# Kernel tuning notes

Measured on AMD Instinct MI355X. Metric: run time of the kernel, lower is better.

The kernel has to match this reference:

```python
import jax, jax.numpy as jnp
import numpy as np

# Model dims (match init_kwargs)
H = 16        # num query heads
HKV = 4       # num key/value heads
D = 128       # head dim
HID = H * D   # hidden size = 2048
W = 4         # ring world size; we simulate rank W-1 (sees all kv shards)
SL = 2048     # local (per-rank) sequence length


def _block_attn(q, kb, vb, scale, causal):
    # q: [B,H,Sl,D], kb/vb: [B,H,Sl,D]
    S = jnp.einsum('bhqd,bhkd->bhqk', q, kb) * scale
    if causal:
        mask = jnp.triu(jnp.ones((q.shape[2], kb.shape[2]), dtype=bool), k=1)
        S = jnp.where(mask[None, None], -jnp.inf, S)
    S_max = jnp.max(S, axis=-1, keepdims=True)
    exp_S = jnp.exp(S - S_max)
    exp_sum = jnp.sum(exp_S, axis=-1, keepdims=True)
    lse = jnp.log(exp_sum) + S_max            # [B,H,Sl,1]
    O = jnp.einsum('bhqk,bhkd->bhqd', exp_S / exp_sum, vb)
    return O, lse


def _ring_attention_fwd(x_q, x_kv, Wq, Wk, Wv, Wo):
    B, Sl, hid = x_q.shape
    n_rep = H // HKV
    scale = 1.0 / np.sqrt(D).astype(np.float32)

    q = (x_q @ Wq.T).reshape(B, Sl, H, D).transpose(0, 2, 1, 3)          # [B,H,Sl,D]
    k = (x_kv @ Wk.T).reshape(B, -1, HKV, D).transpose(0, 2, 1, 3)       # [B,Hkv,Stot,D]
    v = (x_kv @ Wv.T).reshape(B, -1, HKV, D).transpose(0, 2, 1, 3)
    # repeat_kv (GQA)
    k = jnp.repeat(k, n_rep, axis=1)                                     # [B,H,Stot,D]
    v = jnp.repeat(v, n_rep, axis=1)
    # split kv into W ring shards along sequence
    kb = k.reshape(B, H, W, Sl, D)
    vb = v.reshape(B, H, W, Sl, D)

    out, lse = None, None
    rank = W - 1
    for step in range(W):  # fixed small ring loop
        blk = rank - step  # shard held at this ring step (own shard first)
        bo, blse = _block_attn(q, kb[:, :, blk], vb[:, :, blk], scale, causal=(step == 0))
        if out is None:
            out, lse = bo, blse
        else:
            # online merge (matches update_out_and_lse)
            out = out - jax.nn.sigmoid(blse - lse) * (out - bo)
            lse = lse - jax.nn.log_sigmoid(lse - blse)

    out = out.transpose(0, 2, 1, 3).reshape(B, Sl, H * D)
    return out @ Wo.T


def setup_inputs() -> dict:
    key = jax.random.key(0)
    ks = jax.random.split(key, 6)
    s = 0.02
    return {
        'x_q': jax.random.normal(ks[0], (1, SL, HID), dtype=jnp.float32),
        'x_kv': jax.random.normal(ks[1], (1, W * SL, HID), dtype=jnp.float32),
        'Wq': jax.random.normal(ks[2], (HID, HID), dtype=jnp.float32) * s,
        'Wk': jax.random.normal(ks[3], (HKV * D, HID), dtype=jnp.float32) * s,
        'Wv': jax.random.normal(ks[4], (HKV * D, HID), dtype=jnp.float32) * s,
        'Wo': jax.random.normal(ks[5], (HID, HID), dtype=jnp.float32) * s,
    }


def reference(x_q, x_kv, Wq, Wk, Wv, Wo):
    return _ring_attention_fwd(x_q, x_kv, Wq, Wk, Wv, Wo)
```

## Files before the change

kernel.cpp:

```cpp
#include <hip/hip_runtime.h>
#include <stdint.h>

typedef unsigned short u16;
typedef short bf16x8 __attribute__((ext_vector_type(8)));
typedef float f32x4 __attribute__((ext_vector_type(4)));

#define MFMA16(a, b, c) __builtin_amdgcn_mfma_f32_16x16x32_bf16(a, b, c, 0, 0, 0)

__device__ __forceinline__ void ld_lds16(const void* g, void* l) {
  __builtin_amdgcn_global_load_lds(
      (const __attribute__((address_space(1))) void*)(uint64_t)(uintptr_t)g,
      (__attribute__((address_space(3))) void*)(uint32_t)(uintptr_t)l,
      16, 0, 0);
}

__device__ __forceinline__ u16 f32_to_bf16(float f) {
  uint32_t u = __float_as_uint(f);
  return (u16)((u + 0x7FFFu + ((u >> 16) & 1u)) >> 16);
}

__device__ __forceinline__ uint32_t cvt_pk_bf16(float a, float b) {
  uint32_t r;
  asm("v_cvt_pk_bf16_f32 %0, %1, %2" : "=v"(r) : "v"(a), "v"(b));
  return r;
}

__global__ void cvt_all(const float* __restrict__ xq, const float* __restrict__ xkv,
                        const float* __restrict__ Wq, const float* __restrict__ Wk,
                        const float* __restrict__ Wv, const float* __restrict__ Wo,
                        u16* __restrict__ xq_b, u16* __restrict__ xkv_b,
                        u16* __restrict__ wq_b, u16* __restrict__ wk_b,
                        u16* __restrict__ wv_b, u16* __restrict__ wo_b) {
  const int M4 = 1 << 20;
  const int total = 7 * M4 + (M4 >> 1);
  int i = blockIdx.x * blockDim.x + threadIdx.x;
  int stride = gridDim.x * blockDim.x;
  for (; i < total; i += stride) {
    const float* src;
    u16* dst;
    int off;
    if (i < M4)                         { src = xq;  dst = xq_b;  off = i; }
    else if (i < 5 * M4)                { src = xkv; dst = xkv_b; off = i - M4; }
    else if (i < 6 * M4)                { src = Wq;  dst = wq_b;  off = i - 5 * M4; }
    else if (i < 6 * M4 + (M4 >> 2))    { src = Wk;  dst = wk_b;  off = i - 6 * M4; }
    else if (i < 6 * M4 + (M4 >> 1))    { src = Wv;  dst = wv_b;  off = i - 6 * M4 - (M4 >> 2); }
    else                                { src = Wo;  dst = wo_b;  off = i - 6 * M4 - (M4 >> 1); }
    float4 v = reinterpret_cast<const float4*>(src)[off];
    ushort4 o;
    o.x = f32_to_bf16(v.x); o.y = f32_to_bf16(v.y);
    o.z = f32_to_bf16(v.z); o.w = f32_to_bf16(v.w);
    reinterpret_cast<ushort4*>(dst)[off] = o;
  }
}

__device__ __forceinline__ void gemm_body(const u16* __restrict__ A,
                                          const u16* __restrict__ B,
                                          void* __restrict__ Cv, int M, int N,
                                          int K, float alpha, int bx, int by,
                                          int outf32, u16* lA, u16* lB) {
  const int tid = threadIdx.x;
  const int lane = tid & 63;
  const int w = tid >> 6;
  const int c = lane & 15, g = lane >> 4;
  const int wm = (w & 1) * 64, wn = (w >> 1) * 32;
  const int m0 = by * 128, n0 = bx * 64;
  const int sr = tid >> 3, sc = tid & 7;

  f32x4 acc[4][2] = {};

  for (int k0 = 0; k0 < K; k0 += 64) {
    __syncthreads();
#pragma unroll
    for (int p = 0; p < 4; ++p) {
      int row = p * 32 + sr;
      int gc = sc ^ (row & 7);
      ld_lds16(A + (size_t)(m0 + row) * K + k0 + gc * 8, &lA[row * 64 + sc * 8]);
    }
#pragma unroll
    for (int p = 0; p < 2; ++p) {
      int idx = p * 256 + tid;
      int row = idx >> 3, cc = idx & 7;
      int gc = cc ^ (row & 7);
      ld_lds16(B + (size_t)(n0 + row) * K + k0 + gc * 8, &lB[row * 64 + cc * 8]);
    }
    __syncthreads();
#pragma unroll
    for (int kc = 0; kc < 2; ++kc) {
      bf16x8 a[4], b[2];
#pragma unroll
      for (int t = 0; t < 4; ++t) {
        int row = wm + t * 16 + c;
        int ch = (g + 4 * kc) ^ (row & 7);
        a[t] = *(const bf16x8*)&lA[row * 64 + ch * 8];
      }
#pragma unroll
      for (int t = 0; t < 2; ++t) {
        int row = wn + t * 16 + c;
        int ch = (g + 4 * kc) ^ (row & 7);
        b[t] = *(const bf16x8*)&lB[row * 64 + ch * 8];
      }
#pragma unroll
      for (int i = 0; i < 4; ++i)
#pragma unroll
        for (int j = 0; j < 2; ++j)
          acc[i][j] = MFMA16(a[i], b[j], acc[i][j]);
    }
  }

#pragma unroll
  for (int i = 0; i < 4; ++i)
#pragma unroll
    for (int j = 0; j < 2; ++j)
#pragma unroll
      for (int r = 0; r < 4; ++r) {
        int mm = m0 + wm + i * 16 + g * 4 + r;
        int nn = n0 + wn + j * 16 + c;
        float v = acc[i][j][r] * alpha;
        if (outf32)
          ((float*)Cv)[(size_t)mm * N + nn] = v;
        else
          ((u16*)Cv)[(size_t)mm * N + nn] = f32_to_bf16(v);
      }
}

__global__ __launch_bounds__(256, 4)
void gemm3(const u16* __restrict__ xq_b, const u16* __restrict__ wq_b,
           u16* __restrict__ Qb, const u16* __restrict__ xkv_b,
           const u16* __restrict__ wk_b, u16* __restrict__ Kb,
           const u16* __restrict__ wv_b, u16* __restrict__ VTb, float qscale) {
  __shared__ u16 lA[128 * 64];
  __shared__ u16 lB[64 * 64];
  int b = blockIdx.x;
  if (b < 512) {
    gemm_body(xq_b, wq_b, Qb, 2048, 2048, 2048, qscale, b & 31, b >> 5, 0, lA, lB);
  } else if (b < 1024) {
    b -= 512;
    gemm_body(xkv_b, wk_b, Kb, 8192, 512, 2048, 1.0f, b & 7, b >> 3, 0, lA, lB);
  } else {
    b -= 1024;
    gemm_body(wv_b, xkv_b, VTb, 512, 8192, 2048, 1.0f, b & 127, b >> 7, 0, lA, lB);
  }
}

__global__ __launch_bounds__(256, 4)
void gemm_out(const u16* __restrict__ A, const u16* __restrict__ B,
              float* __restrict__ Cv) {
  __shared__ u16 lA[128 * 64];
  __shared__ u16 lB[64 * 64];
  gemm_body(A, B, Cv, 2048, 2048, 2048, 1.0f, blockIdx.x, blockIdx.y, 1, lA, lB);
}

__global__ __launch_bounds__(256, 2)
void attn_kernel(const u16* __restrict__ Q, const u16* __restrict__ Kg,
                 const u16* __restrict__ VT, float* __restrict__ Opart,
                 float* __restrict__ mlp) {
  __shared__ u16 lK[2][64 * 128];
  __shared__ u16 lV[2][128 * 64];
  __shared__ uint32_t lP32[4][16 * 36];

  const int tid = threadIdx.x;
  const int w = tid >> 6, lane = tid & 63;
  const int c = lane & 15, g = lane >> 4;
  const int bx = blockIdx.x;
  const int h = bx & 15, qb = (bx >> 4) & 15, kvs = bx >> 8;
  const int hk = h >> 2;
  const int i0 = qb * 128;
  const int q0 = i0 + w * 32;

  const int nt = ((i0 + 6271) >> 6) + 1;
  const int nth = nt >> 1;
  const int t0 = kvs ? nth : 0;
  const int ntt = (kvs ? nt : nth) - t0;

  bf16x8 qf0[4], qf1[4];
#pragma unroll
  for (int kc = 0; kc < 4; ++kc) {
    qf0[kc] = *(const bf16x8*)&Q[(size_t)(q0 + c) * 2048 + h * 128 + kc * 32 + g * 8];
    qf1[kc] = *(const bf16x8*)&Q[(size_t)(q0 + 16 + c) * 2048 + h * 128 + kc * 32 + g * 8];
  }

  f32x4 a0[8] = {}, a1[8] = {};
  float m0s = -1e30f, l0s = 0.f, m1s = -1e30f, l1s = 0.f;

  auto stage = [&](int buf, int t) {
    const int j0 = t << 6;
#pragma unroll
    for (int p = 0; p < 4; ++p) {
      int idx = p * 256 + tid;
      int row = idx >> 4, cc = idx & 15;
      int gc = cc ^ (row & 15);
      ld_lds16(Kg + (size_t)(j0 + row) * 512 + hk * 128 + gc * 8,
               &lK[buf][row * 128 + cc * 8]);
    }
#pragma unroll
    for (int p = 0; p < 4; ++p) {
      int idx = p * 256 + tid;
      int row = idx >> 3, cc = idx & 7;
      int gc = cc ^ (row & 7);
      ld_lds16(VT + (size_t)(hk * 128 + row) * 8192 + j0 + gc * 8,
               &lV[buf][row * 64 + cc * 8]);
    }
  };

  uint32_t* lPw = &lP32[w][0];

  auto softmax_pb = [&](f32x4 (&sm)[4], float& ms, float& ls, f32x4 (&av)[8],
                        bf16x8 (&pb)[2]) {
    float tm = sm[0][0];
#pragma unroll
    for (int jt = 0; jt < 4; ++jt)
#pragma unroll
      for (int r = 0; r < 4; ++r) tm = fmaxf(tm, sm[jt][r]);
    tm = fmaxf(tm, __shfl_xor(tm, 16));
    tm = fmaxf(tm, __shfl_xor(tm, 32));
    if (!__all(tm - ms <= 8.0f)) {
      float mnew = fmaxf(ms, tm);
      float al = exp2f(ms - mnew);
      ls *= al; ms = mnew;
#pragma unroll
      for (int dt = 0; dt < 8; ++dt) av[dt] *= al;
    }
    float p_[4][4];
    float ps = 0.f;
#pragma unroll
    for (int jt = 0; jt < 4; ++jt)
#pragma unroll
      for (int r = 0; r < 4; ++r) {
        p_[jt][r] = exp2f(sm[jt][r] - ms);
        ps += p_[jt][r];
      }
    ps += __shfl_xor(ps, 16);
    ps += __shfl_xor(ps, 32);
    ls += ps;
#pragma unroll
    for (int jt = 0; jt < 4; ++jt) {
      lPw[c * 36 + jt * 8 + g * 2 + 0] = cvt_pk_bf16(p_[jt][0], p_[jt][1]);
      lPw[c * 36 + jt * 8 + g * 2 + 1] = cvt_pk_bf16(p_[jt][2], p_[jt][3]);
    }
    pb[0] = *(const bf16x8*)&lPw[c * 36 + g * 4];
    pb[1] = *(const bf16x8*)&lPw[c * 36 + 16 + g * 4];
  };

  stage(0, t0);

  for (int it = 0; it < ntt; ++it) {
    const int curb = it & 1;
    const int j0 = (t0 + it) << 6;
    if (it + 1 < ntt) {
      stage(curb ^ 1, t0 + it + 1);
      asm volatile("s_waitcnt vmcnt(8)" ::: "memory");
    } else {
      asm volatile("s_waitcnt vmcnt(0)" ::: "memory");
    }
    __builtin_amdgcn_s_barrier();

    f32x4 s0[4] = {}, s1[4] = {};
    __builtin_amdgcn_s_setprio(1);
#pragma unroll
    for (int kc = 0; kc < 4; ++kc)
#pragma unroll
      for (int jt = 0; jt < 4; ++jt) {
        int row = jt * 16 + c;
        int ch = (g + 4 * kc) ^ (row & 15);
        bf16x8 kf = *(const bf16x8*)&lK[curb][row * 128 + ch * 8];
        s0[jt] = MFMA16(kf, qf0[kc], s0[jt]);
        s1[jt] = MFMA16(kf, qf1[kc], s1[jt]);
      }
    __builtin_amdgcn_s_setprio(0);

    if (j0 + 63 > q0 + 6144) {
#pragma unroll
      for (int jt = 0; jt < 4; ++jt)
#pragma unroll
        for (int r = 0; r < 4; ++r) {
          int jg = j0 + jt * 16 + g * 4 + r;
          if (jg > q0 + c + 6144) s0[jt][r] = -1e30f;
          if (jg > q0 + 16 + c + 6144) s1[jt][r] = -1e30f;
        }
    }

    bf16x8 pb0[2], pb1[2];
    softmax_pb(s0, m0s, l0s, a0, pb0);
    softmax_pb(s1, m1s, l1s, a1, pb1);

    __builtin_amdgcn_s_setprio(1);
#pragma unroll
    for (int dt = 0; dt < 8; ++dt)
#pragma unroll
      for (int kc2 = 0; kc2 < 2; ++kc2) {
        int row = dt * 16 + c;
        int vch = (g + 4 * kc2) ^ (row & 7);
        bf16x8 vf = *(const bf16x8*)&lV[curb][row * 64 + vch * 8];
        a0[dt] = MFMA16(vf, pb0[kc2], a0[dt]);
        a1[dt] = MFMA16(vf, pb1[kc2], a1[dt]);
      }
    __builtin_amdgcn_s_setprio(0);

    __builtin_amdgcn_s_barrier();
  }

  const size_t pbase = ((size_t)(kvs * 16 + h) * 16 + qb);
  float* Op = Opart + pbase * 16384;
  float* mlb = mlp + pbase * 256;
  const int qi0 = w * 32 + c;
#pragma unroll
  for (int dt = 0; dt < 8; ++dt) {
    *(f32x4*)&Op[(size_t)qi0 * 128 + dt * 16 + g * 4] = a0[dt];
    *(f32x4*)&Op[(size_t)(qi0 + 16) * 128 + dt * 16 + g * 4] = a1[dt];
  }
  if (g == 0) {
    mlb[qi0] = m0s;
    mlb[128 + qi0] = l0s;
    mlb[qi0 + 16] = m1s;
    mlb[128 + qi0 + 16] = l1s;
  }
}

__global__ __launch_bounds__(256)
void attn_merge(const float* __restrict__ Opart, const float* __restrict__ mlp,
                u16* __restrict__ O) {
  const int bx = blockIdx.x;
  const int h = bx >> 4, qb = bx & 15;
  const int q = threadIdx.x & 127, hf = threadIdx.x >> 7;
  const size_t p0 = ((size_t)(0 + h) * 16 + qb);
  const size_t p1 = ((size_t)(16 + h) * 16 + qb);
  float mm0 = mlp[p0 * 256 + q], ll0 = mlp[p0 * 256 + 128 + q];
  float mm1 = mlp[p1 * 256 + q], ll1 = mlp[p1 * 256 + 128 + q];
  float m = fmaxf(mm0, mm1);
  float w0 = exp2f(mm0 - m), w1 = exp2f(mm1 - m);
  float inv = 1.f / (ll0 * w0 + ll1 * w1);
  const float* A = Opart + p0 * 16384 + (size_t)q * 128 + hf * 64;
  const float* B = Opart + p1 * 16384 + (size_t)q * 128 + hf * 64;
  u16* out = O + (size_t)(qb * 128 + q) * 2048 + h * 128 + hf * 64;
#pragma unroll
  for (int d = 0; d < 64; d += 4) {
    float4 a = *(const float4*)&A[d];
    float4 b = *(const float4*)&B[d];
    ushort4 o;
    o.x = f32_to_bf16((a.x * w0 + b.x * w1) * inv);
    o.y = f32_to_bf16((a.y * w0 + b.y * w1) * inv);
    o.z = f32_to_bf16((a.z * w0 + b.z * w1) * inv);
    o.w = f32_to_bf16((a.w * w0 + b.w * w1) * inv);
    *(ushort4*)&out[d] = o;
  }
}

extern "C" void kernel_launch(void* const* d_in, const int* in_sizes, int n_in,
                              void* d_out, int out_size, void* d_ws, size_t ws_size,
                              hipStream_t stream) {
  (void)in_sizes; (void)n_in; (void)out_size; (void)ws_size;
  const float* xq = (const float*)d_in[0];
  const float* xkv = (const float*)d_in[1];
  const float* Wq = (const float*)d_in[2];
  const float* Wk = (const float*)d_in[3];
  const float* Wv = (const float*)d_in[4];
  const float* Wo = (const float*)d_in[5];

  u16* ws = (u16*)d_ws;
  const size_t M1 = 1024 * 1024;
  u16* xq_b  = ws;
  u16* xkv_b = ws + 4 * M1;
  u16* wq_b  = ws + 20 * M1;
  u16* wk_b  = ws + 24 * M1;
  u16* wv_b  = ws + 25 * M1;
  u16* wo_b  = ws + 26 * M1;
  u16* Qb    = ws + 30 * M1;
  u16* Kb    = ws + 34 * M1;
  u16* VTb   = ws + 38 * M1;
  u16* Ob    = ws + 42 * M1;
  float* Opart = (float*)d_ws;
  float* mlptr = Opart + 8388608;

  cvt_all<<<2048, 256, 0, stream>>>(xq, xkv, Wq, Wk, Wv, Wo,
                                    xq_b, xkv_b, wq_b, wk_b, wv_b, wo_b);

  gemm3<<<1536, 256, 0, stream>>>(xq_b, wq_b, Qb, xkv_b, wk_b, Kb, wv_b, VTb,
                                  0.12752837f);

  attn_kernel<<<512, 256, 0, stream>>>(Qb, Kb, VTb, Opart, mlptr);
  attn_merge<<<256, 256, 0, stream>>>(Opart, mlptr, Ob);

  gemm_out<<<dim3(32, 16), 256, 0, stream>>>(Ob, wo_b, (float*)d_out);
}
```

Baseline: 324.5 us.

## Split attention KV range three ways and read V fragments directly from global

The KV tile range of each attention block is now split into three parts instead of two. That raises the grid from 512 to 768 blocks, and the merge kernel is generalised to a three-way weighted combine. The V tile no longer goes through LDS: each lane loads its V^T fragment straight from global memory inside the PV MFMA loop. This cuts LDS use and lets launch bounds rise to 3 blocks per CU. The trade is that V reads become latency-exposed global/L2 loads in the inner loop, and there is more partial-output traffic to write and merge.

Result: slower. 489.4 us (+50.8%).

```diff
diff --git a/kernel.cpp b/kernel.cpp
--- a/kernel.cpp
+++ b/kernel.cpp
@@ -150,12 +150,11 @@
   gemm_body(A, B, Cv, 2048, 2048, 2048, 1.0f, blockIdx.x, blockIdx.y, 1, lA, lB);
 }
 
-__global__ __launch_bounds__(256, 2)
+__global__ __launch_bounds__(256, 3)
 void attn_kernel(const u16* __restrict__ Q, const u16* __restrict__ Kg,
                  const u16* __restrict__ VT, float* __restrict__ Opart,
                  float* __restrict__ mlp) {
   __shared__ u16 lK[2][64 * 128];
-  __shared__ u16 lV[2][128 * 64];
   __shared__ uint32_t lP32[4][16 * 36];
 
   const int tid = threadIdx.x;
@@ -168,9 +167,9 @@
   const int q0 = i0 + w * 32;
 
   const int nt = ((i0 + 6271) >> 6) + 1;
-  const int nth = nt >> 1;
-  const int t0 = kvs ? nth : 0;
-  const int ntt = (kvs ? nt : nth) - t0;
+  const int t0 = (nt * kvs) / 3;
+  const int t1 = (nt * (kvs + 1)) / 3;
+  const int ntt = t1 - t0;
 
   bf16x8 qf0[4], qf1[4];
 #pragma unroll
@@ -181,6 +180,8 @@
 
   f32x4 a0[8] = {}, a1[8] = {};
   float m0s = -1e30f, l0s = 0.f, m1s = -1e30f, l1s = 0.f;
+
+  const u16* Vrow = VT + (size_t)(hk * 128 + c) * 8192;
 
   auto stage = [&](int buf, int t) {
     const int j0 = t << 6;
@@ -191,14 +192,6 @@
       int gc = cc ^ (row & 15);
       ld_lds16(Kg + (size_t)(j0 + row) * 512 + hk * 128 + gc * 8,
                &lK[buf][row * 128 + cc * 8]);
-    }
-#pragma unroll
-    for (int p = 0; p < 4; ++p) {
-      int idx = p * 256 + tid;
-      int row = idx >> 3, cc = idx & 7;
-      int gc = cc ^ (row & 7);
-      ld_lds16(VT + (size_t)(hk * 128 + row) * 8192 + j0 + gc * 8,
-               &lV[buf][row * 64 + cc * 8]);
     }
   };
 
@@ -248,7 +241,7 @@
     const int j0 = (t0 + it) << 6;
     if (it + 1 < ntt) {
       stage(curb ^ 1, t0 + it + 1);
-      asm volatile("s_waitcnt vmcnt(8)" ::: "memory");
+      asm volatile("s_waitcnt vmcnt(4)" ::: "memory");
     } else {
       asm volatile("s_waitcnt vmcnt(0)" ::: "memory");
     }
@@ -288,9 +281,7 @@
     for (int dt = 0; dt < 8; ++dt)
 #pragma unroll
       for (int kc2 = 0; kc2 < 2; ++kc2) {
-        int row = dt * 16 + c;
-        int vch = (g + 4 * kc2) ^ (row & 7);
-        bf16x8 vf = *(const bf16x8*)&lV[curb][row * 64 + vch * 8];
+        bf16x8 vf = *(const bf16x8*)&Vrow[(size_t)dt * 16 * 8192 + j0 + kc2 * 32 + g * 8];
         a0[dt] = MFMA16(vf, pb0[kc2], a0[dt]);
         a1[dt] = MFMA16(vf, pb1[kc2], a1[dt]);
       }
@@ -322,25 +313,41 @@
   const int bx = blockIdx.x;
   const int h = bx >> 4, qb = bx & 15;
   const int q = threadIdx.x & 127, hf = threadIdx.x >> 7;
-  const size_t p0 = ((size_t)(0 + h) * 16 + qb);
-  const size_t p1 = ((size_t)(16 + h) * 16 + qb);
-  float mm0 = mlp[p0 * 256 + q], ll0 = mlp[p0 * 256 + 128 + q];
-  float mm1 = mlp[p1 * 256 + q], ll1 = mlp[p1 * 256 + 128 + q];
-  float m = fmaxf(mm0, mm1);
-  float w0 = exp2f(mm0 - m), w1 = exp2f(mm1 - m);
-  float inv = 1.f / (ll0 * w0 + ll1 * w1);
-  const float* A = Opart + p0 * 16384 + (size_t)q * 128 + hf * 64;
-  const float* B = Opart + p1 * 16384 + (size_t)q * 128 + hf * 64;
+
+  float ms[3], ls[3], m = -1e30f;
+#pragma unroll
+  for (int s = 0; s < 3; ++s) {
+    size_t pidx = ((size_t)(s * 16 + h) * 16 + qb);
+    ms[s] = mlp[pidx * 256 + q];
+    ls[s] = mlp[pidx * 256 + 128 + q];
+    m = fmaxf(m, ms[s]);
+  }
+  float wgt[3], denom = 0.f;
+#pragma unroll
+  for (int s = 0; s < 3; ++s) {
+    wgt[s] = exp2f(ms[s] - m);
+    denom += ls[s] * wgt[s];
+  }
+  float inv = 1.f / denom;
+
   u16* out = O + (size_t)(qb * 128 + q) * 2048 + h * 128 + hf * 64;
 #pragma unroll
   for (int d = 0; d < 64; d += 4) {
-    float4 a = *(const float4*)&A[d];
-    float4 b = *(const float4*)&B[d];
+    float acc0 = 0.f, acc1 = 0.f, acc2 = 0.f, acc3 = 0.f;
+#pragma unroll
+    for (int s = 0; s < 3; ++s) {
+      size_t pidx = ((size_t)(s * 16 + h) * 16 + qb);
+      float4 a = *(const float4*)&Opart[pidx * 16384 + (size_t)q * 128 + hf * 64 + d];
+      acc0 += wgt[s] * a.x;
+      acc1 += wgt[s] * a.y;
+      acc2 += wgt[s] * a.z;
+      acc3 += wgt[s] * a.w;
+    }
     ushort4 o;
-    o.x = f32_to_bf16((a.x * w0 + b.x * w1) * inv);
-    o.y = f32_to_bf16((a.y * w0 + b.y * w1) * inv);
-    o.z = f32_to_bf16((a.z * w0 + b.z * w1) * inv);
-    o.w = f32_to_bf16((a.w * w0 + b.w * w1) * inv);
+    o.x = f32_to_bf16(acc0 * inv);
+    o.y = f32_to_bf16(acc1 * inv);
+    o.z = f32_to_bf16(acc2 * inv);
+    o.w = f32_to_bf16(acc3 * inv);
     *(ushort4*)&out[d] = o;
   }
 }
@@ -369,7 +376,7 @@
   u16* VTb   = ws + 38 * M1;
   u16* Ob    = ws + 42 * M1;
   float* Opart = (float*)d_ws;
-  float* mlptr = Opart + 8388608;
+  float* mlptr = Opart + 12582912;
 
   cvt_all<<<2048, 256, 0, stream>>>(xq, xkv, Wq, Wk, Wv, Wo,
                                     xq_b, xkv_b, wq_b, wk_b, wv_b, wo_b);
@@ -377,7 +384,7 @@
   gemm3<<<1536, 256, 0, stream>>>(xq_b, wq_b, Qb, xkv_b, wk_b, Kb, wv_b, VTb,
                                   0.12752837f);
 
-  attn_kernel<<<512, 256, 0, stream>>>(Qb, Kb, VTb, Opart, mlptr);
+  attn_kernel<<<768, 256, 0, stream>>>(Qb, Kb, VTb, Opart, mlptr);
   attn_merge<<<256, 256, 0, stream>>>(Opart, mlptr, Ob);
 
   gemm_out<<<dim3(32, 16), 256, 0, stream>>>(Ob, wo_b, (float*)d_out);
```
